# Performance work log

Measured on AMD Instinct MI355X. Metric: run time of the kernel, lower is better.

Reference implementation:

```python
import jax, jax.numpy as jnp
import numpy as np

B, S, H = 2, 1024, 2048
E, K, F = 64, 8, 768
CAP = 512


def setup_inputs() -> dict:
    key = jax.random.key(0)
    k1, k2, k3, k4, k5 = jax.random.split(key, 5)
    scale_h = 1.0 / np.sqrt(H)
    scale_f = 1.0 / np.sqrt(F)
    return {
        "hidden_states": jax.random.normal(k1, (B, S, H), jnp.float32),
        "router_w": jax.random.normal(k2, (E, H), jnp.float32) * scale_h,   # MoEGate.weight [E, H]
        "w_gate": jax.random.normal(k3, (E, H, F), jnp.float32) * scale_h,
        "w_up": jax.random.normal(k4, (E, H, F), jnp.float32) * scale_h,
        "w_down": jax.random.normal(k5, (E, F, H), jnp.float32) * scale_f,
    }


def reference(hidden_states, router_w, w_gate, w_up, w_down):
    b, s, h = hidden_states.shape
    T = b * s
    xf = hidden_states.reshape(T, h)

    # --- MoEGate: softmax over expert logits, then top-k, then renormalize ---
    logits = xf @ router_w.T                                   # [T, E]
    scores = jax.nn.softmax(logits.astype(jnp.float32), axis=-1)
    topk_w, topk_idx = jax.lax.top_k(scores, K)                # [T, K]
    topk_w = topk_w / (topk_w.sum(axis=-1, keepdims=True) + 1e-20)

    # --- dispatch: scatter each (token, k) slot into a per-expert capacity buffer ---
    slot_expert = topk_idx.reshape(-1)                         # [T*K]
    slot_token = jnp.repeat(jnp.arange(T), K)                  # [T*K]
    onehot = jax.nn.one_hot(slot_expert, E, dtype=jnp.int32)   # [T*K, E]
    pos = (jnp.cumsum(onehot, axis=0) * onehot).sum(-1) - 1    # position within expert
    valid = pos < CAP
    dest = jnp.where(valid, slot_expert * CAP + pos, E * CAP)  # overflow -> dummy row

    buf = jnp.zeros((E * CAP + 1, h), xf.dtype).at[dest].set(xf[slot_token])
    xb = buf[: E * CAP].reshape(E, CAP, h)                     # [E, CAP, H]

    # --- grouped GEMM experts: SwiGLU MLP per expert ---
    gate = jnp.einsum("ech,ehf->ecf", xb, w_gate)
    up = jnp.einsum("ech,ehf->ecf", xb, w_up)
    hmid = jax.nn.silu(gate) * up                              # [E, CAP, F]
    yb = jnp.einsum("ecf,efh->ech", hmid, w_down).reshape(E * CAP, h)
    yb = jnp.concatenate([yb, jnp.zeros((1, h), yb.dtype)], axis=0)

    # --- combine: gather expert outputs back, weight, scatter-add per token ---
    slot_out = yb[dest] * topk_w.reshape(-1)[:, None].astype(yb.dtype)
    out = jnp.zeros((T, h), yb.dtype).at[slot_token].add(slot_out)
    return out.reshape(b, s, h)
```

## Files before the change

### kernel.cpp

```cpp
#include <hip/hip_runtime.h>
#include <math.h>

#define T_TOK 2048
#define HD    2048
#define NEXP  64
#define KTOP  8
#define FD    768
#define CAPE  512

typedef float  f32x4 __attribute__((ext_vector_type(4)));
typedef __bf16 bf16x8 __attribute__((ext_vector_type(8)));
typedef __bf16 bf16x4 __attribute__((ext_vector_type(4)));

__device__ __forceinline__ void load_lds16(const void* g, void* l) {
  __builtin_amdgcn_global_load_lds(
      (const __attribute__((address_space(1))) unsigned int*)g,
      (__attribute__((address_space(3))) unsigned int*)l, 16, 0, 0);
}

#define WAITCNT(S) asm volatile(S ::: "memory")
#define BARRIER()  __builtin_amdgcn_s_barrier()

__global__ __launch_bounds__(256) void router_kernel(
    const float* __restrict__ x, const float* __restrict__ rw,
    int* __restrict__ cnt, int* __restrict__ tok_list, float* __restrict__ w_list)
{
  const int t = threadIdx.x;
  const int tb = blockIdx.x * 4;
  __shared__ float xs[4][HD];
  __shared__ float lg[4][NEXP];

  const float4* xsrc = (const float4*)(x + (size_t)tb * HD);
  float4* xdst = (float4*)&xs[0][0];
  for (int i = t; i < 4 * HD / 4; i += 256) xdst[i] = xsrc[i];
  __syncthreads();

  {
    const int e = t >> 2, q = t & 3;
    const float* wrow = rw + (size_t)e * HD;
    float a0 = 0.f, a1 = 0.f, a2 = 0.f, a3 = 0.f;
    for (int i = 0; i < HD / 16; ++i) {
      int h = (i * 4 + q) * 4;
      float4 wv = *(const float4*)(wrow + h);
      float4 x0 = *(const float4*)&xs[0][h];
      float4 x1 = *(const float4*)&xs[1][h];
      float4 x2 = *(const float4*)&xs[2][h];
      float4 x3 = *(const float4*)&xs[3][h];
      a0 += wv.x*x0.x + wv.y*x0.y + wv.z*x0.z + wv.w*x0.w;
      a1 += wv.x*x1.x + wv.y*x1.y + wv.z*x1.z + wv.w*x1.w;
      a2 += wv.x*x2.x + wv.y*x2.y + wv.z*x2.z + wv.w*x2.w;
      a3 += wv.x*x3.x + wv.y*x3.y + wv.z*x3.z + wv.w*x3.w;
    }
    a0 += __shfl_xor(a0, 1); a0 += __shfl_xor(a0, 2);
    a1 += __shfl_xor(a1, 1); a1 += __shfl_xor(a1, 2);
    a2 += __shfl_xor(a2, 1); a2 += __shfl_xor(a2, 2);
    a3 += __shfl_xor(a3, 1); a3 += __shfl_xor(a3, 2);
    if (q == 0) { lg[0][e] = a0; lg[1][e] = a1; lg[2][e] = a2; lg[3][e] = a3; }
  }
  __syncthreads();

  const int wid = t >> 6, lane = t & 63;
  float v = lg[wid][lane];
  float mx = v;
  for (int o = 32; o; o >>= 1) mx = fmaxf(mx, __shfl_xor(mx, o));
  float p = expf(v - mx);
  float s = p;
  for (int o = 32; o; o >>= 1) s += __shfl_xor(s, o);
  float prob = p / s;

  float r = prob;
  float wk[KTOP]; int ik[KTOP]; float wsum = 0.f;
  #pragma unroll
  for (int k = 0; k < KTOP; ++k) {
    float bv = r; int bl = lane;
    for (int o = 32; o; o >>= 1) {
      float ov = __shfl_xor(bv, o); int ol = __shfl_xor(bl, o);
      if (ov > bv || (ov == bv && ol < bl)) { bv = ov; bl = ol; }
    }
    wk[k] = bv; ik[k] = bl; wsum += bv;
    if (lane == bl) r = -1.f;
  }
  if (lane == 0) {
    float inv = 1.f / (wsum + 1e-20f);
    int token = tb + wid;
    #pragma unroll
    for (int k = 0; k < KTOP; ++k) {
      int ex = ik[k];
      int pos = atomicAdd(&cnt[ex], 1);
      if (pos < CAPE) {
        tok_list[ex * CAPE + pos] = token;
        w_list[ex * CAPE + pos] = wk[k] * inv;
      }
    }
  }
}

__global__ __launch_bounds__(256) void cvt_kernel(
    const float* __restrict__ x, unsigned short* __restrict__ xb)
{
  int i = blockIdx.x * 256 + threadIdx.x;
  f32x4 v = ((const f32x4*)x)[i];
  bf16x4 o = { (__bf16)v[0], (__bf16)v[1], (__bf16)v[2], (__bf16)v[3] };
  ((bf16x4*)xb)[i] = o;
}


__global__ __launch_bounds__(256, 2) void gateup_kernel(
    const unsigned short* __restrict__ xb,
    const float* __restrict__ wg, const float* __restrict__ wu,
    const int* __restrict__ cnt, const int* __restrict__ tok_list,
    unsigned short* __restrict__ hmid)
{
  const int nt = blockIdx.x, mt = blockIdx.y, e = blockIdx.z;
  int ne = cnt[e]; ne = ne < CAPE ? ne : CAPE;
  if (mt * 128 >= ne) return;
  const int t = threadIdx.x, lane = t & 63, wid = t >> 6;
  const int wr = wid >> 1, wc = wid & 1;

  __shared__ __align__(16) unsigned short A[2 * 128 * 64];
  __shared__ __align__(16) unsigned short Bg[2 * 64 * 72];
  __shared__ __align__(16) unsigned short Bu[2 * 64 * 72];
  __shared__ int toks[128];

  if (t < 128) {
    int r = mt * 128 + t;
    toks[t] = tok_list[e * CAPE + (r < ne ? r : 0)];
  }
  __syncthreads();

  const unsigned short* asrc[4];
  #pragma unroll
  for (int i = 0; i < 4; ++i) {
    const int inst = wid * 4 + i;
    const int G = inst * 64 + lane;
    const int m = G >> 3, gg = G & 7;
    asrc[i] = xb + (size_t)toks[m] * HD + 8 * (gg ^ (m & 7));
  }

  f32x4 z4 = {0.f, 0.f, 0.f, 0.f};
  f32x4 gacc[4][2], uacc[4][2];
  #pragma unroll
  for (int i = 0; i < 4; ++i)
    #pragma unroll
    for (int j = 0; j < 2; ++j) { gacc[i][j] = z4; uacc[i][j] = z4; }

  const size_t wbase = (size_t)e * HD * FD + (size_t)nt * 64;
  const int nc = t & 15, kc = t >> 4;
  f32x4 Ra[8], Rb[8];

#define LOAD_GU(K0, R) do { \
    const float* pg_ = wg + wbase + (size_t)((K0) + kc * 4) * FD + nc * 4; \
    const float* pu_ = wu + wbase + (size_t)((K0) + kc * 4) * FD + nc * 4; \
    R[0] = *(const f32x4*)pg_;            R[1] = *(const f32x4*)(pg_ + FD); \
    R[2] = *(const f32x4*)(pg_ + 2*FD);   R[3] = *(const f32x4*)(pg_ + 3*FD); \
    R[4] = *(const f32x4*)pu_;            R[5] = *(const f32x4*)(pu_ + FD); \
    R[6] = *(const f32x4*)(pu_ + 2*FD);   R[7] = *(const f32x4*)(pu_ + 3*FD); \
  } while (0)

#define STAGE_A4(KT, BUF) do { \
    const int k0s_ = (KT) * 64; \
    _Pragma("unroll") \
    for (int i_ = 0; i_ < 4; ++i_) \
      load_lds16(asrc[i_] + k0s_, &A[(BUF) * 8192 + (wid * 4 + i_) * 512]); \
  } while (0)

#define CVT_GU(BUF, R) do { \
    __bf16* bg_ = (__bf16*)&Bg[(BUF) * 4608]; \
    __bf16* bu_ = (__bf16*)&Bu[(BUF) * 4608]; \
    const int xm_ = (nc & 7) << 3; \
    _Pragma("unroll") \
    for (int j_ = 0; j_ < 4; ++j_) { \
      int so_ = (nc * 4 + j_) * 72 + ((kc * 4) ^ xm_); \
      *(bf16x4*)&bg_[so_] = (bf16x4){(__bf16)R[0][j_], (__bf16)R[1][j_], (__bf16)R[2][j_], (__bf16)R[3][j_]}; \
      *(bf16x4*)&bu_[so_] = (bf16x4){(__bf16)R[4][j_], (__bf16)R[5][j_], (__bf16)R[6][j_], (__bf16)R[7][j_]}; \
    } \
  } while (0)

#define COMPUTE_GU(CUR) do { \
    const char* Ab_ = (const char*)&A[(CUR) * 8192]; \
    const __bf16* Bg_ = (const __bf16*)&Bg[(CUR) * 4608]; \
    const __bf16* Bu_ = (const __bf16*)&Bu[(CUR) * 4608]; \
    _Pragma("unroll") \
    for (int ks = 0; ks < 2; ++ks) { \
      bf16x8 af[4]; \
      _Pragma("unroll") \
      for (int mf = 0; mf < 4; ++mf) { \
        int row = wr * 64 + mf * 16 + (lane & 15); \
        int byte = row * 128 + (lane >> 4) * 16 + ks * 64; \
        byte ^= (row & 7) << 4; \
        af[mf] = *(const bf16x8*)(Ab_ + byte); \
      } \
      _Pragma("unroll") \
      for (int nf = 0; nf < 2; ++nf) { \
        int n = wc * 32 + nf * 16 + (lane & 15); \
        int so = n * 72 + ((((lane >> 4) * 8) + ks * 32) ^ (((n >> 2) & 7) << 3)); \
        bf16x8 bgf = *(const bf16x8*)&Bg_[so]; \
        bf16x8 bum = *(const bf16x8*)&Bu_[so]; \
        _Pragma("unroll") \
        for (int mf = 0; mf < 4; ++mf) { \
          gacc[mf][nf] = __builtin_amdgcn_mfma_f32_16x16x32_bf16(af[mf], bgf, gacc[mf][nf], 0, 0, 0); \
          uacc[mf][nf] = __builtin_amdgcn_mfma_f32_16x16x32_bf16(af[mf], bum, uacc[mf][nf], 0, 0, 0); \
        } \
      } \
    } \
  } while (0)

  LOAD_GU(0, Ra);
  STAGE_A4(0, 0);
  LOAD_GU(64, Rb);
  WAITCNT("s_waitcnt vmcnt(12)");
  CVT_GU(0, Ra);
  WAITCNT("s_waitcnt vmcnt(8) lgkmcnt(0)");
  BARRIER();

  for (int i = 0; i < 15; ++i) {
    const int kt = 2 * i;
    STAGE_A4(kt + 1, 1);
    LOAD_GU((kt + 2) * 64, Ra);
    WAITCNT("s_waitcnt vmcnt(12)");
    CVT_GU(1, Rb);
    COMPUTE_GU(0);
    WAITCNT("s_waitcnt vmcnt(8) lgkmcnt(0)");
    BARRIER();

    STAGE_A4(kt + 2, 0);
    LOAD_GU((kt + 3) * 64, Rb);
    WAITCNT("s_waitcnt vmcnt(12)");
    CVT_GU(0, Ra);
    COMPUTE_GU(1);
    WAITCNT("s_waitcnt vmcnt(8) lgkmcnt(0)");
    BARRIER();
  }
  STAGE_A4(31, 1);
  CVT_GU(1, Rb);
  COMPUTE_GU(0);
  WAITCNT("s_waitcnt vmcnt(0) lgkmcnt(0)");
  BARRIER();
  COMPUTE_GU(1);

#undef LOAD_GU
#undef STAGE_A4
#undef CVT_GU
#undef COMPUTE_GU

  const size_t hbase = (size_t)e * CAPE + (size_t)mt * 128;
  __bf16* hm = (__bf16*)hmid;
  #pragma unroll
  for (int mf = 0; mf < 4; ++mf) {
    #pragma unroll
    for (int nf = 0; nf < 2; ++nf) {
      #pragma unroll
      for (int r = 0; r < 4; ++r) {
        int row = wr * 64 + mf * 16 + (lane >> 4) * 4 + r;
        int c = nt * 64 + wc * 32 + nf * 16 + (lane & 15);
        float gv = gacc[mf][nf][r], uv = uacc[mf][nf][r];
        float hv = gv / (1.f + __expf(-gv)) * uv;
        hm[(hbase + row) * FD + c] = (__bf16)hv;
      }
    }
  }
}

__global__ __launch_bounds__(256, 2) void down_kernel(
    const unsigned short* __restrict__ hmid,
    const float* __restrict__ wd,
    const int* __restrict__ cnt, const int* __restrict__ tok_list,
    const float* __restrict__ w_list, float* __restrict__ out)
{
  const int nt = blockIdx.x, mt = blockIdx.y, e = blockIdx.z;
  int ne = cnt[e]; ne = ne < CAPE ? ne : CAPE;
  if (mt * 128 >= ne) return;
  const int t = threadIdx.x, lane = t & 63, wid = t >> 6;
  const int wr = wid >> 1, wc = wid & 1;

  __shared__ __align__(16) unsigned short A[2 * 128 * 64];
  __shared__ __align__(16) unsigned short Bd[2 * 64 * 72];
  __shared__ int toks[128];
  __shared__ float wts[128];

  if (t < 128) {
    int r = mt * 128 + t;
    bool vv = r < ne;
    toks[t] = vv ? tok_list[e * CAPE + r] : 0;
    wts[t]  = vv ? w_list[e * CAPE + r] : 0.f;
  }
  __syncthreads();

  const size_t arow = (size_t)e * CAPE + (size_t)mt * 128;
  const unsigned short* asrc[4];
  #pragma unroll
  for (int i = 0; i < 4; ++i) {
    const int inst = wid * 4 + i;
    const int G = inst * 64 + lane;
    const int m = G >> 3, gg = G & 7;
    asrc[i] = hmid + (arow + m) * FD + 8 * (gg ^ (m & 7));
  }

  f32x4 z4 = {0.f, 0.f, 0.f, 0.f};
  f32x4 dacc[4][2];
  #pragma unroll
  for (int i = 0; i < 4; ++i)
    #pragma unroll
    for (int j = 0; j < 2; ++j) dacc[i][j] = z4;

  const size_t wbase = (size_t)e * FD * HD + (size_t)nt * 64;
  const int nc = t & 15, kc = t >> 4;
  f32x4 Ra[4], Rb[4];

#define LOAD_D(K0, R) do { \
    const float* pd_ = wd + wbase + (size_t)((K0) + kc * 4) * HD + nc * 4; \
    R[0] = *(const f32x4*)pd_;            R[1] = *(const f32x4*)(pd_ + HD); \
    R[2] = *(const f32x4*)(pd_ + 2*HD);   R[3] = *(const f32x4*)(pd_ + 3*HD); \
  } while (0)

#define STAGE_A4(KT, BUF) do { \
    const int k0s_ = (KT) * 64; \
    _Pragma("unroll") \
    for (int i_ = 0; i_ < 4; ++i_) \
      load_lds16(asrc[i_] + k0s_, &A[(BUF) * 8192 + (wid * 4 + i_) * 512]); \
  } while (0)

#define CVT_D(BUF, R) do { \
    __bf16* bd_ = (__bf16*)&Bd[(BUF) * 4608]; \
    const int xm_ = (nc & 7) << 3; \
    _Pragma("unroll") \
    for (int j_ = 0; j_ < 4; ++j_) { \
      int so_ = (nc * 4 + j_) * 72 + ((kc * 4) ^ xm_); \
      *(bf16x4*)&bd_[so_] = (bf16x4){(__bf16)R[0][j_], (__bf16)R[1][j_], (__bf16)R[2][j_], (__bf16)R[3][j_]}; \
    } \
  } while (0)

#define COMPUTE_D(CUR) do { \
    const char* Ab_ = (const char*)&A[(CUR) * 8192]; \
    const __bf16* Bd_ = (const __bf16*)&Bd[(CUR) * 4608]; \
    _Pragma("unroll") \
    for (int ks = 0; ks < 2; ++ks) { \
      bf16x8 af[4]; \
      _Pragma("unroll") \
      for (int mf = 0; mf < 4; ++mf) { \
        int row = wr * 64 + mf * 16 + (lane & 15); \
        int byte = row * 128 + (lane >> 4) * 16 + ks * 64; \
        byte ^= (row & 7) << 4; \
        af[mf] = *(const bf16x8*)(Ab_ + byte); \
      } \
      _Pragma("unroll") \
      for (int nf = 0; nf < 2; ++nf) { \
        int n = wc * 32 + nf * 16 + (lane & 15); \
        int so = n * 72 + ((((lane >> 4) * 8) + ks * 32) ^ (((n >> 2) & 7) << 3)); \
        bf16x8 bdf = *(const bf16x8*)&Bd_[so]; \
        _Pragma("unroll") \
        for (int mf = 0; mf < 4; ++mf) \
          dacc[mf][nf] = __builtin_amdgcn_mfma_f32_16x16x32_bf16(af[mf], bdf, dacc[mf][nf], 0, 0, 0); \
      } \
    } \
  } while (0)

  LOAD_D(0, Ra);
  STAGE_A4(0, 0);
  LOAD_D(64, Rb);
  WAITCNT("s_waitcnt vmcnt(8)");
  CVT_D(0, Ra);
  WAITCNT("s_waitcnt vmcnt(4) lgkmcnt(0)");
  BARRIER();

  for (int i = 0; i < 5; ++i) {
    const int kt = 2 * i;
    STAGE_A4(kt + 1, 1);
    LOAD_D((kt + 2) * 64, Ra);
    WAITCNT("s_waitcnt vmcnt(8)");
    CVT_D(1, Rb);
    COMPUTE_D(0);
    WAITCNT("s_waitcnt vmcnt(4) lgkmcnt(0)");
    BARRIER();

    STAGE_A4(kt + 2, 0);
    LOAD_D((kt + 3) * 64, Rb);
    WAITCNT("s_waitcnt vmcnt(8)");
    CVT_D(0, Ra);
    COMPUTE_D(1);
    WAITCNT("s_waitcnt vmcnt(4) lgkmcnt(0)");
    BARRIER();
  }
  STAGE_A4(11, 1);
  CVT_D(1, Rb);
  COMPUTE_D(0);
  WAITCNT("s_waitcnt vmcnt(0) lgkmcnt(0)");
  BARRIER();
  COMPUTE_D(1);

#undef LOAD_D
#undef STAGE_A4
#undef CVT_D
#undef COMPUTE_D

  #pragma unroll
  for (int mf = 0; mf < 4; ++mf) {
    #pragma unroll
    for (int nf = 0; nf < 2; ++nf) {
      int c = nt * 64 + wc * 32 + nf * 16 + (lane & 15);
      #pragma unroll
      for (int r = 0; r < 4; ++r) {
        int row = wr * 64 + mf * 16 + (lane >> 4) * 4 + r;
        if (mt * 128 + row < ne) {
          int tok = toks[row];
          float w = wts[row];
          atomicAdd(&out[(size_t)tok * HD + c], w * dacc[mf][nf][r]);
        }
      }
    }
  }
}

extern "C" void kernel_launch(void* const* d_in, const int* in_sizes, int n_in,
                              void* d_out, int out_size, void* d_ws, size_t ws_size,
                              hipStream_t stream) {
  const float* x  = (const float*)d_in[0];
  const float* rw = (const float*)d_in[1];
  const float* wg = (const float*)d_in[2];
  const float* wu = (const float*)d_in[3];
  const float* wd = (const float*)d_in[4];
  float* out = (float*)d_out;

  char* ws = (char*)d_ws;
  unsigned short* xb   = (unsigned short*)ws;
  int* cnt             = (int*)(ws + 8388608);
  int* tok_list        = (int*)(ws + 8388864);
  float* w_list        = (float*)(ws + 8519936);
  unsigned short* hmid = (unsigned short*)(ws + 8651008);

  hipMemsetAsync(d_out, 0, (size_t)out_size * sizeof(float), stream);
  hipMemsetAsync(cnt, 0, NEXP * sizeof(int), stream);

  router_kernel<<<T_TOK / 4, 256, 0, stream>>>(x, rw, cnt, tok_list, w_list);
  cvt_kernel<<<(T_TOK * HD / 4) / 256, 256, 0, stream>>>(x, xb);
  gateup_kernel<<<dim3(FD / 64, CAPE / 128, NEXP), 256, 0, stream>>>(xb, wg, wu, cnt, tok_list, hmid);
  down_kernel<<<dim3(HD / 64, CAPE / 128, NEXP), 256, 0, stream>>>(hmid, wd, cnt, tok_list, w_list, out);
}
```

Before: 654.2 us.

## Single-buffer B tiles in LDS for 3 blocks/CU and fuse bf16 cast into router

The B-operand LDS tile in the gate/up and down GEMM kernels goes from double to single buffering. Compute now runs before the register-to-LDS conversion, separated by an extra barrier, and launch bounds rise from 2 to 3 blocks per CU for more occupancy and latency hiding. The separate fp32-to-bf16 conversion kernel is removed and the cast is folded into the router kernel, which saves a launch and a re-read of x. The cost is an extra barrier per k-step, and compute can no longer overlap the next B tile's LDS stores, which may stall the MFMA pipeline.

```diff
diff --git a/kernel.cpp b/kernel.cpp
--- a/kernel.cpp
+++ b/kernel.cpp
@@ -23,7 +23,8 @@
 
 __global__ __launch_bounds__(256) void router_kernel(
     const float* __restrict__ x, const float* __restrict__ rw,
-    int* __restrict__ cnt, int* __restrict__ tok_list, float* __restrict__ w_list)
+    int* __restrict__ cnt, int* __restrict__ tok_list, float* __restrict__ w_list,
+    unsigned short* __restrict__ xb)
 {
   const int t = threadIdx.x;
   const int tb = blockIdx.x * 4;
@@ -57,6 +58,16 @@
     a3 += __shfl_xor(a3, 1); a3 += __shfl_xor(a3, 2);
     if (q == 0) { lg[0][e] = a0; lg[1][e] = a1; lg[2][e] = a2; lg[3][e] = a3; }
   }
+
+  {
+    const f32x4* xs4 = (const f32x4*)(x + (size_t)tb * HD);
+    bf16x4* xbd = (bf16x4*)(xb + (size_t)tb * HD);
+    #pragma unroll
+    for (int j = 0; j < 8; ++j) {
+      f32x4 v = xs4[j * 256 + t];
+      xbd[j * 256 + t] = (bf16x4){(__bf16)v[0], (__bf16)v[1], (__bf16)v[2], (__bf16)v[3]};
+    }
+  }
   __syncthreads();
 
   const int wid = t >> 6, lane = t & 63;
@@ -95,17 +106,8 @@
   }
 }
 
-__global__ __launch_bounds__(256) void cvt_kernel(
-    const float* __restrict__ x, unsigned short* __restrict__ xb)
-{
-  int i = blockIdx.x * 256 + threadIdx.x;
-  f32x4 v = ((const f32x4*)x)[i];
-  bf16x4 o = { (__bf16)v[0], (__bf16)v[1], (__bf16)v[2], (__bf16)v[3] };
-  ((bf16x4*)xb)[i] = o;
-}
-
-
-__global__ __launch_bounds__(256, 2) void gateup_kernel(
+
+__global__ __launch_bounds__(256, 3) void gateup_kernel(
     const unsigned short* __restrict__ xb,
     const float* __restrict__ wg, const float* __restrict__ wu,
     const int* __restrict__ cnt, const int* __restrict__ tok_list,
@@ -118,8 +120,8 @@
   const int wr = wid >> 1, wc = wid & 1;
 
   __shared__ __align__(16) unsigned short A[2 * 128 * 64];
-  __shared__ __align__(16) unsigned short Bg[2 * 64 * 72];
-  __shared__ __align__(16) unsigned short Bu[2 * 64 * 72];
+  __shared__ __align__(16) unsigned short Bg[64 * 72];
+  __shared__ __align__(16) unsigned short Bu[64 * 72];
   __shared__ int toks[128];
 
   if (t < 128) {
@@ -164,9 +166,9 @@
       load_lds16(asrc[i_] + k0s_, &A[(BUF) * 8192 + (wid * 4 + i_) * 512]); \
   } while (0)
 
-#define CVT_GU(BUF, R) do { \
-    __bf16* bg_ = (__bf16*)&Bg[(BUF) * 4608]; \
-    __bf16* bu_ = (__bf16*)&Bu[(BUF) * 4608]; \
+#define CVT_GU(R) do { \
+    __bf16* bg_ = (__bf16*)Bg; \
+    __bf16* bu_ = (__bf16*)Bu; \
     const int xm_ = (nc & 7) << 3; \
     _Pragma("unroll") \
     for (int j_ = 0; j_ < 4; ++j_) { \
@@ -178,8 +180,8 @@
 
 #define COMPUTE_GU(CUR) do { \
     const char* Ab_ = (const char*)&A[(CUR) * 8192]; \
-    const __bf16* Bg_ = (const __bf16*)&Bg[(CUR) * 4608]; \
-    const __bf16* Bu_ = (const __bf16*)&Bu[(CUR) * 4608]; \
+    const __bf16* Bg_ = (const __bf16*)Bg; \
+    const __bf16* Bu_ = (const __bf16*)Bu; \
     _Pragma("unroll") \
     for (int ks = 0; ks < 2; ++ks) { \
       bf16x8 af[4]; \
@@ -209,7 +211,7 @@
   STAGE_A4(0, 0);
   LOAD_GU(64, Rb);
   WAITCNT("s_waitcnt vmcnt(12)");
-  CVT_GU(0, Ra);
+  CVT_GU(Ra);
   WAITCNT("s_waitcnt vmcnt(8) lgkmcnt(0)");
   BARRIER();
 
@@ -217,23 +219,30 @@
     const int kt = 2 * i;
     STAGE_A4(kt + 1, 1);
     LOAD_GU((kt + 2) * 64, Ra);
+    COMPUTE_GU(0);
+    WAITCNT("s_waitcnt lgkmcnt(0)");
+    BARRIER();
     WAITCNT("s_waitcnt vmcnt(12)");
-    CVT_GU(1, Rb);
-    COMPUTE_GU(0);
+    CVT_GU(Rb);
     WAITCNT("s_waitcnt vmcnt(8) lgkmcnt(0)");
     BARRIER();
 
     STAGE_A4(kt + 2, 0);
     LOAD_GU((kt + 3) * 64, Rb);
+    COMPUTE_GU(1);
+    WAITCNT("s_waitcnt lgkmcnt(0)");
+    BARRIER();
     WAITCNT("s_waitcnt vmcnt(12)");
-    CVT_GU(0, Ra);
-    COMPUTE_GU(1);
+    CVT_GU(Ra);
     WAITCNT("s_waitcnt vmcnt(8) lgkmcnt(0)");
     BARRIER();
   }
   STAGE_A4(31, 1);
-  CVT_GU(1, Rb);
   COMPUTE_GU(0);
+  WAITCNT("s_waitcnt lgkmcnt(0)");
+  BARRIER();
+  WAITCNT("s_waitcnt vmcnt(4)");
+  CVT_GU(Rb);
   WAITCNT("s_waitcnt vmcnt(0) lgkmcnt(0)");
   BARRIER();
   COMPUTE_GU(1);
@@ -261,7 +270,7 @@
   }
 }
 
-__global__ __launch_bounds__(256, 2) void down_kernel(
+__global__ __launch_bounds__(256, 3) void down_kernel(
     const unsigned short* __restrict__ hmid,
     const float* __restrict__ wd,
     const int* __restrict__ cnt, const int* __restrict__ tok_list,
@@ -274,7 +283,7 @@
   const int wr = wid >> 1, wc = wid & 1;
 
   __shared__ __align__(16) unsigned short A[2 * 128 * 64];
-  __shared__ __align__(16) unsigned short Bd[2 * 64 * 72];
+  __shared__ __align__(16) unsigned short Bd[64 * 72];
   __shared__ int toks[128];
   __shared__ float wts[128];
 
@@ -320,8 +329,8 @@
       load_lds16(asrc[i_] + k0s_, &A[(BUF) * 8192 + (wid * 4 + i_) * 512]); \
   } while (0)
 
-#define CVT_D(BUF, R) do { \
-    __bf16* bd_ = (__bf16*)&Bd[(BUF) * 4608]; \
+#define CVT_D(R) do { \
+    __bf16* bd_ = (__bf16*)Bd; \
     const int xm_ = (nc & 7) << 3; \
     _Pragma("unroll") \
     for (int j_ = 0; j_ < 4; ++j_) { \
@@ -332,7 +341,7 @@
 
 #define COMPUTE_D(CUR) do { \
     const char* Ab_ = (const char*)&A[(CUR) * 8192]; \
-    const __bf16* Bd_ = (const __bf16*)&Bd[(CUR) * 4608]; \
+    const __bf16* Bd_ = (const __bf16*)Bd; \
     _Pragma("unroll") \
     for (int ks = 0; ks < 2; ++ks) { \
       bf16x8 af[4]; \
@@ -359,7 +368,7 @@
   STAGE_A4(0, 0);
   LOAD_D(64, Rb);
   WAITCNT("s_waitcnt vmcnt(8)");
-  CVT_D(0, Ra);
+  CVT_D(Ra);
   WAITCNT("s_waitcnt vmcnt(4) lgkmcnt(0)");
   BARRIER();
 
@@ -367,23 +376,30 @@
     const int kt = 2 * i;
     STAGE_A4(kt + 1, 1);
     LOAD_D((kt + 2) * 64, Ra);
+    COMPUTE_D(0);
+    WAITCNT("s_waitcnt lgkmcnt(0)");
+    BARRIER();
     WAITCNT("s_waitcnt vmcnt(8)");
-    CVT_D(1, Rb);
-    COMPUTE_D(0);
+    CVT_D(Rb);
     WAITCNT("s_waitcnt vmcnt(4) lgkmcnt(0)");
     BARRIER();
 
     STAGE_A4(kt + 2, 0);
     LOAD_D((kt + 3) * 64, Rb);
+    COMPUTE_D(1);
+    WAITCNT("s_waitcnt lgkmcnt(0)");
+    BARRIER();
     WAITCNT("s_waitcnt vmcnt(8)");
-    CVT_D(0, Ra);
-    COMPUTE_D(1);
+    CVT_D(Ra);
     WAITCNT("s_waitcnt vmcnt(4) lgkmcnt(0)");
     BARRIER();
   }
   STAGE_A4(11, 1);
-  CVT_D(1, Rb);
   COMPUTE_D(0);
+  WAITCNT("s_waitcnt lgkmcnt(0)");
+  BARRIER();
+  WAITCNT("s_waitcnt vmcnt(4)");
+  CVT_D(Rb);
   WAITCNT("s_waitcnt vmcnt(0) lgkmcnt(0)");
   BARRIER();
   COMPUTE_D(1);
@@ -431,8 +447,7 @@
   hipMemsetAsync(d_out, 0, (size_t)out_size * sizeof(float), stream);
   hipMemsetAsync(cnt, 0, NEXP * sizeof(int), stream);
 
-  router_kernel<<<T_TOK / 4, 256, 0, stream>>>(x, rw, cnt, tok_list, w_list);
-  cvt_kernel<<<(T_TOK * HD / 4) / 256, 256, 0, stream>>>(x, xb);
+  router_kernel<<<T_TOK / 4, 256, 0, stream>>>(x, rw, cnt, tok_list, w_list, xb);
   gateup_kernel<<<dim3(FD / 64, CAPE / 128, NEXP), 256, 0, stream>>>(xb, wg, wu, cnt, tok_list, hmid);
   down_kernel<<<dim3(HD / 64, CAPE / 128, NEXP), 256, 0, stream>>>(hmid, wd, cnt, tok_list, w_list, out);
 }
```

Result: slower. 893.5 us (+36.6%).

## Deepen weight prefetch to three register stages and fuse bf16 cast into router

Applied to the files above, without the earlier changes.

The gate/up and down GEMM kernels now keep three register buffers of fp32 weight loads in flight instead of two. Wait counts are raised so the global-load latency is hidden over two compute steps, and compiler memory barriers pin the issue order. The separate fp32-to-bf16 conversion kernel is removed and folded into the router kernel, saving one launch and one extra pass over the activations. The cost is more VGPRs per thread, which could reduce occupancy under launch_bounds(256,2) or cause spills.

```diff
diff --git a/kernel.cpp b/kernel.cpp
--- a/kernel.cpp
+++ b/kernel.cpp
@@ -19,11 +19,13 @@
 }
 
 #define WAITCNT(S) asm volatile(S ::: "memory")
+#define PIN()      asm volatile("" ::: "memory")
 #define BARRIER()  __builtin_amdgcn_s_barrier()
 
 __global__ __launch_bounds__(256) void router_kernel(
     const float* __restrict__ x, const float* __restrict__ rw,
-    int* __restrict__ cnt, int* __restrict__ tok_list, float* __restrict__ w_list)
+    int* __restrict__ cnt, int* __restrict__ tok_list, float* __restrict__ w_list,
+    unsigned short* __restrict__ xb)
 {
   const int t = threadIdx.x;
   const int tb = blockIdx.x * 4;
@@ -57,6 +59,16 @@
     a3 += __shfl_xor(a3, 1); a3 += __shfl_xor(a3, 2);
     if (q == 0) { lg[0][e] = a0; lg[1][e] = a1; lg[2][e] = a2; lg[3][e] = a3; }
   }
+
+  {
+    const f32x4* xs4 = (const f32x4*)(x + (size_t)tb * HD);
+    bf16x4* xbd = (bf16x4*)(xb + (size_t)tb * HD);
+    #pragma unroll
+    for (int j = 0; j < 8; ++j) {
+      f32x4 v = xs4[j * 256 + t];
+      xbd[j * 256 + t] = (bf16x4){(__bf16)v[0], (__bf16)v[1], (__bf16)v[2], (__bf16)v[3]};
+    }
+  }
   __syncthreads();
 
   const int wid = t >> 6, lane = t & 63;
@@ -94,16 +106,6 @@
     }
   }
 }
-
-__global__ __launch_bounds__(256) void cvt_kernel(
-    const float* __restrict__ x, unsigned short* __restrict__ xb)
-{
-  int i = blockIdx.x * 256 + threadIdx.x;
-  f32x4 v = ((const f32x4*)x)[i];
-  bf16x4 o = { (__bf16)v[0], (__bf16)v[1], (__bf16)v[2], (__bf16)v[3] };
-  ((bf16x4*)xb)[i] = o;
-}
-
 
 __global__ __launch_bounds__(256, 2) void gateup_kernel(
     const unsigned short* __restrict__ xb,
@@ -146,7 +148,7 @@
 
   const size_t wbase = (size_t)e * HD * FD + (size_t)nt * 64;
   const int nc = t & 15, kc = t >> 4;
-  f32x4 Ra[8], Rb[8];
+  f32x4 Ra[8], Rb[8], Rc[8];
 
 #define LOAD_GU(K0, R) do { \
     const float* pg_ = wg + wbase + (size_t)((K0) + kc * 4) * FD + nc * 4; \
@@ -205,33 +207,40 @@
     } \
   } while (0)
 
-  LOAD_GU(0, Ra);
-  STAGE_A4(0, 0);
-  LOAD_GU(64, Rb);
+#define STEP_GU(KT, RCVT, RLOAD) do { \
+    STAGE_A4((KT) + 1, ((KT) + 1) & 1);  PIN(); \
+    LOAD_GU(((KT) + 3) * 64, RLOAD);     PIN(); \
+    WAITCNT("s_waitcnt vmcnt(20)"); \
+    CVT_GU(((KT) + 1) & 1, RCVT); \
+    COMPUTE_GU((KT) & 1); \
+    WAITCNT("s_waitcnt vmcnt(16) lgkmcnt(0)"); \
+    BARRIER(); \
+  } while (0)
+
+  LOAD_GU(0, Ra);            PIN();
+  STAGE_A4(0, 0);            PIN();
+  LOAD_GU(64, Rb);           PIN();
+  LOAD_GU(128, Rc);          PIN();
+  WAITCNT("s_waitcnt vmcnt(20)");
+  CVT_GU(0, Ra);
+  WAITCNT("s_waitcnt vmcnt(16) lgkmcnt(0)");
+  BARRIER();
+
+  for (int i = 0; i < 9; ++i) {
+    const int kt = 3 * i;
+    STEP_GU(kt + 0, Rb, Ra);
+    STEP_GU(kt + 1, Rc, Rb);
+    STEP_GU(kt + 2, Ra, Rc);
+  }
+  STEP_GU(27, Rb, Ra);
+  STEP_GU(28, Rc, Rb);
+  STAGE_A4(30, 0);  PIN();
   WAITCNT("s_waitcnt vmcnt(12)");
   CVT_GU(0, Ra);
-  WAITCNT("s_waitcnt vmcnt(8) lgkmcnt(0)");
-  BARRIER();
-
-  for (int i = 0; i < 15; ++i) {
-    const int kt = 2 * i;
-    STAGE_A4(kt + 1, 1);
-    LOAD_GU((kt + 2) * 64, Ra);
-    WAITCNT("s_waitcnt vmcnt(12)");
-    CVT_GU(1, Rb);
-    COMPUTE_GU(0);
-    WAITCNT("s_waitcnt vmcnt(8) lgkmcnt(0)");
-    BARRIER();
-
-    STAGE_A4(kt + 2, 0);
-    LOAD_GU((kt + 3) * 64, Rb);
-    WAITCNT("s_waitcnt vmcnt(12)");
-    CVT_GU(0, Ra);
-    COMPUTE_GU(1);
-    WAITCNT("s_waitcnt vmcnt(8) lgkmcnt(0)");
-    BARRIER();
-  }
-  STAGE_A4(31, 1);
+  COMPUTE_GU(1);
+  WAITCNT("s_waitcnt vmcnt(0) lgkmcnt(0)");
+  BARRIER();
+  STAGE_A4(31, 1);  PIN();
   CVT_GU(1, Rb);
   COMPUTE_GU(0);
   WAITCNT("s_waitcnt vmcnt(0) lgkmcnt(0)");
@@ -242,6 +251,7 @@
 #undef STAGE_A4
 #undef CVT_GU
 #undef COMPUTE_GU
+#undef STEP_GU
 
   const size_t hbase = (size_t)e * CAPE + (size_t)mt * 128;
   __bf16* hm = (__bf16*)hmid;
@@ -305,7 +315,7 @@
 
   const size_t wbase = (size_t)e * FD * HD + (size_t)nt * 64;
   const int nc = t & 15, kc = t >> 4;
-  f32x4 Ra[4], Rb[4];
+  f32x4 Ra[4], Rb[4], Rc[4];
 
 #define LOAD_D(K0, R) do { \
     const float* pd_ = wd + wbase + (size_t)((K0) + kc * 4) * HD + nc * 4; \
@@ -355,34 +365,39 @@
     } \
   } while (0)
 
-  LOAD_D(0, Ra);
-  STAGE_A4(0, 0);
-  LOAD_D(64, Rb);
+#define STEP_D(KT, RCVT, RLOAD) do { \
+    STAGE_A4((KT) + 1, ((KT) + 1) & 1);  PIN(); \
+    LOAD_D(((KT) + 3) * 64, RLOAD);      PIN(); \
+    WAITCNT("s_waitcnt vmcnt(12)"); \
+    CVT_D(((KT) + 1) & 1, RCVT); \
+    COMPUTE_D((KT) & 1); \
+    WAITCNT("s_waitcnt vmcnt(8) lgkmcnt(0)"); \
+    BARRIER(); \
+  } while (0)
+
+  LOAD_D(0, Ra);            PIN();
+  STAGE_A4(0, 0);           PIN();
+  LOAD_D(64, Rb);           PIN();
+  LOAD_D(128, Rc);          PIN();
+  WAITCNT("s_waitcnt vmcnt(12)");
+  CVT_D(0, Ra);
+  WAITCNT("s_waitcnt vmcnt(8) lgkmcnt(0)");
+  BARRIER();
+
+  for (int i = 0; i < 3; ++i) {
+    const int kt = 3 * i;
+    STEP_D(kt + 0, Rb, Ra);
+    STEP_D(kt + 1, Rc, Rb);
+    STEP_D(kt + 2, Ra, Rc);
+  }
+  STAGE_A4(10, 0);  PIN();
   WAITCNT("s_waitcnt vmcnt(8)");
-  CVT_D(0, Ra);
-  WAITCNT("s_waitcnt vmcnt(4) lgkmcnt(0)");
-  BARRIER();
-
-  for (int i = 0; i < 5; ++i) {
-    const int kt = 2 * i;
-    STAGE_A4(kt + 1, 1);
-    LOAD_D((kt + 2) * 64, Ra);
-    WAITCNT("s_waitcnt vmcnt(8)");
-    CVT_D(1, Rb);
-    COMPUTE_D(0);
-    WAITCNT("s_waitcnt vmcnt(4) lgkmcnt(0)");
-    BARRIER();
-
-    STAGE_A4(kt + 2, 0);
-    LOAD_D((kt + 3) * 64, Rb);
-    WAITCNT("s_waitcnt vmcnt(8)");
-    CVT_D(0, Ra);
-    COMPUTE_D(1);
-    WAITCNT("s_waitcnt vmcnt(4) lgkmcnt(0)");
-    BARRIER();
-  }
-  STAGE_A4(11, 1);
-  CVT_D(1, Rb);
+  CVT_D(0, Rb);
+  COMPUTE_D(1);
+  WAITCNT("s_waitcnt vmcnt(0) lgkmcnt(0)");
+  BARRIER();
+  STAGE_A4(11, 1);  PIN();
+  CVT_D(1, Rc);
   COMPUTE_D(0);
   WAITCNT("s_waitcnt vmcnt(0) lgkmcnt(0)");
   BARRIER();
@@ -392,6 +407,7 @@
 #undef STAGE_A4
 #undef CVT_D
 #undef COMPUTE_D
+#undef STEP_D
 
   #pragma unroll
   for (int mf = 0; mf < 4; ++mf) {
@@ -431,8 +447,7 @@
   hipMemsetAsync(d_out, 0, (size_t)out_size * sizeof(float), stream);
   hipMemsetAsync(cnt, 0, NEXP * sizeof(int), stream);
 
-  router_kernel<<<T_TOK / 4, 256, 0, stream>>>(x, rw, cnt, tok_list, w_list);
-  cvt_kernel<<<(T_TOK * HD / 4) / 256, 256, 0, stream>>>(x, xb);
+  router_kernel<<<T_TOK / 4, 256, 0, stream>>>(x, rw, cnt, tok_list, w_list, xb);
   gateup_kernel<<<dim3(FD / 64, CAPE / 128, NEXP), 256, 0, stream>>>(xb, wg, wu, cnt, tok_list, hmid);
   down_kernel<<<dim3(HD / 64, CAPE / 128, NEXP), 256, 0, stream>>>(hmid, wd, cnt, tok_list, w_list, out);
 }
```

Result: slower. 679.2 us (+3.8%).
